# Optimization experiments

Measured on AMD Instinct MI355X. Metric: run time of the kernel, lower is better.

## Reference

```python
import jax, jax.numpy as jnp
import numpy as np

B, N, D = 128, 512, 256
NUM_TYPES, NUM_STATS = 6, 8
W_TYPE, W_STATS, W_CORR = 1.0, 1.0, 0.5
LN_EPS = 1e-5


def _mlp_head(x, W1, b1, g, be, W2, b2):
    # Linear -> GELU(exact) -> LayerNorm -> Linear (dropout is identity in eval)
    h = x @ W1 + b1
    h = jax.nn.gelu(h, approximate=False)
    mu = jnp.mean(h, axis=-1, keepdims=True)
    var = jnp.var(h, axis=-1, keepdims=True)
    h = (h - mu) / jnp.sqrt(var + LN_EPS) * g + be
    return h @ W2 + b2


def _masked_mean(x, m):
    m = m.astype(x.dtype)
    return jnp.sum(x * m) / jnp.maximum(jnp.sum(m), 1.0)


def setup_inputs() -> dict:
    key = jax.random.key(0)
    ks = jax.random.split(key, 16)
    s = 1.0 / np.sqrt(D)
    return {
        'column_embeddings': jax.random.normal(ks[0], (B, N, D), jnp.float32),
        'masked_columns': jax.random.uniform(ks[1], (B, N)) < 0.15,
        'type_targets': jax.random.randint(ks[2], (B, N), 0, NUM_TYPES),
        'column_statistics': jax.random.normal(ks[3], (B, N, NUM_STATS), jnp.float32),
        'column_correlations': jax.random.normal(ks[4], (B, N, N), jnp.float32),
        # type head params
        'Wt1': jax.random.normal(ks[5], (D, D), jnp.float32) * s,
        'bt1': jnp.zeros((D,), jnp.float32),
        'gt': jnp.ones((D,), jnp.float32),
        'blt': jnp.zeros((D,), jnp.float32),
        'Wt2': jax.random.normal(ks[6], (D, NUM_TYPES), jnp.float32) * s,
        'bt2': jnp.zeros((NUM_TYPES,), jnp.float32),
        # stats head params
        'Ws1': jax.random.normal(ks[7], (D, D), jnp.float32) * s,
        'bs1': jnp.zeros((D,), jnp.float32),
        'gs': jnp.ones((D,), jnp.float32),
        'bls': jnp.zeros((D,), jnp.float32),
        'Ws2': jax.random.normal(ks[8], (D, NUM_STATS), jnp.float32) * s,
        'bs2': jnp.zeros((NUM_STATS,), jnp.float32),
        # bilinear correlation head (nn.Bilinear(d,d,1) weight [1,d,d] -> [d,d])
        'Wc': jax.random.normal(ks[9], (D, D), jnp.float32) * s,
        'bc': jnp.zeros((), jnp.float32),
    }


def reference(column_embeddings, masked_columns, type_targets, column_statistics,
              column_correlations, Wt1, bt1, gt, blt, Wt2, bt2,
              Ws1, bs1, gs, bls, Ws2, bs2, Wc, bc):
    x = column_embeddings
    m = masked_columns

    type_logits = _mlp_head(x, Wt1, bt1, gt, blt, Wt2, bt2)   # [B,N,6]
    stats_preds = _mlp_head(x, Ws1, bs1, gs, bls, Ws2, bs2)   # [B,N,8]

    # fused bilinear correlation: replaces the O(N^2) python loop
    scores = jnp.einsum('bid,de,bje->bij', x, Wc, x) + bc     # [B,N,N]
    corr = jnp.tanh(scores)
    eye = jnp.eye(N, dtype=bool)
    corr = jnp.where(eye, jnp.ones((), corr.dtype), corr)

    # type loss: masked-mean cross-entropy
    logp = jax.nn.log_softmax(type_logits, axis=-1)
    nll = -jnp.take_along_axis(logp, type_targets[..., None], axis=-1)[..., 0]
    type_loss = _masked_mean(nll, m)

    # stats loss: masked-mean MSE over all stat elements of masked columns
    se = (stats_preds - column_statistics) ** 2
    stats_loss = _masked_mean(se, jnp.broadcast_to(m[:, :, None], se.shape))

    # correlation loss: mask is union over row/col masked columns
    m2 = m[:, :, None] | m[:, None, :]
    corr_loss = _masked_mean((corr - column_correlations) ** 2, m2)

    total = W_TYPE * type_loss + W_STATS * stats_loss + W_CORR * corr_loss
    return total
```

## Files before the change

kernel.cpp:

```cpp
#include <hip/hip_runtime.h>
#include <hip/hip_bf16.h>

#define BB 128
#define NN 512
#define DD 256

typedef __attribute__((ext_vector_type(4))) float f32x4;
typedef __attribute__((ext_vector_type(8))) short s16x8;
typedef __attribute__((ext_vector_type(8))) __bf16 bf16x8;

static __device__ __forceinline__ bf16x8 as_bf(s16x8 v) {
  return __builtin_bit_cast(bf16x8, v);
}

static __device__ __forceinline__ unsigned short f2bf(float f) {
  unsigned u = __builtin_bit_cast(unsigned, f);
  u += 0x7FFFu + ((u >> 16) & 1u);
  return (unsigned short)(u >> 16);
}

static __device__ __forceinline__ float gelu_fast(float h) {
  float z = 1.5957691216057308f * h * (1.0f + 0.044715f * h * h);
  float e = __expf(z);
  float r = __builtin_amdgcn_rcpf(e + 1.0f);
  return h - h * r;
}

__device__ __forceinline__ float wave_sum(float v) {
#pragma unroll
  for (int o = 32; o > 0; o >>= 1) v += __shfl_xor(v, o);
  return v;
}

__global__ void k_init(int* wsi) {
  if (threadIdx.x < 8) wsi[threadIdx.x] = 0;
}

__global__ void k_counts(const int* __restrict__ msk, int* __restrict__ wsi) {
  const int b = blockIdx.x;
  int cnt = 0;
  for (int i = threadIdx.x; i < NN; i += blockDim.x) cnt += (msk[b * NN + i] != 0) ? 1 : 0;
  float s = wave_sum((float)cnt);
  __shared__ float red[4];
  const int lane = threadIdx.x & 63, wv = threadIdx.x >> 6;
  if (lane == 0) red[wv] = s;
  __syncthreads();
  if (threadIdx.x == 0) {
    int k = (int)(red[0] + red[1] + red[2] + red[3] + 0.5f);
    atomicAdd(&wsi[4], k);
    atomicAdd(&wsi[5], NN * NN - (NN - k) * (NN - k));
  }
}

__global__ void k_prep(const float* __restrict__ Wc, const float* __restrict__ Wt1,
                       const float* __restrict__ Ws1, const float* __restrict__ Wt2,
                       const float* __restrict__ Ws2,
                       unsigned short* __restrict__ WcT, unsigned short* __restrict__ Wt1T,
                       unsigned short* __restrict__ Ws1T, unsigned short* __restrict__ Wt2T,
                       unsigned short* __restrict__ Ws2T) {
  int t = blockIdx.x * 256 + threadIdx.x;
  int c = t >> 8, d = t & 255;
  WcT [c * 256 + d] = f2bf(Wc [d * 256 + c]);
  Wt1T[c * 256 + d] = f2bf(Wt1[d * 256 + c]);
  Ws1T[c * 256 + d] = f2bf(Ws1[d * 256 + c]);
  if (c < 16) {
    Wt2T[c * 256 + d] = (c < 6) ? f2bf(Wt2[d * 6 + c]) : (unsigned short)0;
    Ws2T[c * 256 + d] = (c < 8) ? f2bf(Ws2[d * 8 + c]) : (unsigned short)0;
  }
}

__global__ __launch_bounds__(512) void k_heads(
    const float* __restrict__ x, unsigned short* __restrict__ xbf,
    const int* __restrict__ msk,
    const int* __restrict__ tgt, const float* __restrict__ stats,
    const unsigned short* __restrict__ Wt1T, const unsigned short* __restrict__ Ws1T,
    const unsigned short* __restrict__ Wt2T, const unsigned short* __restrict__ Ws2T,
    const float* __restrict__ bt1, const float* __restrict__ bs1,
    const float* __restrict__ gt, const float* __restrict__ gs,
    const float* __restrict__ blt, const float* __restrict__ bls,
    const float* __restrict__ bt2, const float* __restrict__ bs2,
    float* __restrict__ fs)
{
  const int tid = threadIdx.x;
  const int lane = tid & 63, w = tid >> 6;
  const int wm = w & 1, wn = w >> 1;
  const int fr = lane & 15, fg = lane >> 4;
  const int row0 = blockIdx.x * 128;

  __shared__ __align__(16) unsigned short lds_x[128 * 264];
  __shared__ __align__(16) unsigned short pool2[4224];
  __shared__ float lg[128 * 8];
  unsigned short* lds_h  = lds_x;
  unsigned short* lds_w2 = pool2;
  float* red = (float*)pool2;

#pragma unroll
  for (int p = 0; p < 8; ++p) {
    int c = tid + p * 512;
    int r = c >> 5, ch = c & 31;
    const float4* s = (const float4*)&x[(size_t)(row0 + r) * DD + ch * 8];
    float4 v0 = s[0], v1 = s[1];
    uint4 pk;
    pk.x = (unsigned)f2bf(v0.x) | ((unsigned)f2bf(v0.y) << 16);
    pk.y = (unsigned)f2bf(v0.z) | ((unsigned)f2bf(v0.w) << 16);
    pk.z = (unsigned)f2bf(v1.x) | ((unsigned)f2bf(v1.y) << 16);
    pk.w = (unsigned)f2bf(v1.z) | ((unsigned)f2bf(v1.w) << 16);
    *(uint4*)&lds_x[r * 264 + ch * 8] = pk;
    *(uint4*)&xbf[(size_t)(row0 + r) * DD + ch * 8] = pk;
  }
  __syncthreads();

  f32x4 at[4][4], asx[4][4];
#pragma unroll
  for (int i = 0; i < 4; ++i)
#pragma unroll
    for (int j = 0; j < 4; ++j) {
      at[i][j]  = f32x4{0.f, 0.f, 0.f, 0.f};
      asx[i][j] = f32x4{0.f, 0.f, 0.f, 0.f};
    }

#pragma unroll
  for (int ks = 0; ks < 8; ++ks) {
    const int ko = ks * 32 + fg * 8;
    s16x8 af[4], bt_[4], bs_[4];
#pragma unroll
    for (int i = 0; i < 4; ++i)
      af[i] = *(const s16x8*)&lds_x[(wm * 64 + i * 16 + fr) * 264 + ko];
#pragma unroll
    for (int j = 0; j < 4; ++j) {
      bt_[j] = *(const s16x8*)&Wt1T[(size_t)(wn * 64 + j * 16 + fr) * DD + ko];
      bs_[j] = *(const s16x8*)&Ws1T[(size_t)(wn * 64 + j * 16 + fr) * DD + ko];
    }
#pragma unroll
    for (int i = 0; i < 4; ++i)
#pragma unroll
      for (int j = 0; j < 4; ++j) {
        at[i][j]  = __builtin_amdgcn_mfma_f32_16x16x32_bf16(as_bf(af[i]), as_bf(bt_[j]), at[i][j], 0, 0, 0);
        asx[i][j] = __builtin_amdgcn_mfma_f32_16x16x32_bf16(as_bf(af[i]), as_bf(bs_[j]), asx[i][j], 0, 0, 0);
      }
  }

  {
    float sA[16], qA[16];
#pragma unroll
    for (int k = 0; k < 16; ++k) { sA[k] = 0.f; qA[k] = 0.f; }
#pragma unroll
    for (int i = 0; i < 4; ++i)
#pragma unroll
      for (int j = 0; j < 4; ++j) {
        int col = wn * 64 + j * 16 + fr;
        float bb = bt1[col];
#pragma unroll
        for (int r = 0; r < 4; ++r) {
          float h = gelu_fast(at[i][j][r] + bb);
          at[i][j][r] = h;
          sA[i * 4 + r] += h;
          qA[i * 4 + r] += h * h;
        }
      }
#pragma unroll
    for (int o = 1; o < 16; o <<= 1) {
#pragma unroll
      for (int k = 0; k < 16; ++k) {
        sA[k] += __shfl_xor(sA[k], o);
        qA[k] += __shfl_xor(qA[k], o);
      }
    }
    if (fr == 0) {
#pragma unroll
      for (int i = 0; i < 4; ++i)
#pragma unroll
        for (int r = 0; r < 4; ++r) {
          int row = wm * 64 + i * 16 + fg * 4 + r;
          red[row * 8 + wn]     = sA[i * 4 + r];
          red[row * 8 + 4 + wn] = qA[i * 4 + r];
        }
    }
    __syncthreads();
#pragma unroll
    for (int i = 0; i < 4; ++i)
#pragma unroll
      for (int r = 0; r < 4; ++r) {
        int row = wm * 64 + i * 16 + fg * 4 + r;
        float s = red[row * 8 + 0] + red[row * 8 + 1] + red[row * 8 + 2] + red[row * 8 + 3];
        float q = red[row * 8 + 4] + red[row * 8 + 5] + red[row * 8 + 6] + red[row * 8 + 7];
        float mu = s * (1.0f / DD);
        float var = q * (1.0f / DD) - mu * mu;
        float rstd = rsqrtf(var + 1e-5f);
#pragma unroll
        for (int j = 0; j < 4; ++j) {
          int col = wn * 64 + j * 16 + fr;
          float hn = (at[i][j][r] - mu) * rstd * gt[col] + blt[col];
          lds_h[row * 264 + col] = f2bf(hn);
        }
      }
    __syncthreads();
    {
      int r = tid >> 5, ch = tid & 31;
      *(uint4*)&lds_w2[r * 264 + ch * 8] = *(const uint4*)&Wt2T[r * 256 + ch * 8];
    }
    __syncthreads();
    {
      f32x4 a1 = f32x4{0.f, 0.f, 0.f, 0.f};
#pragma unroll
      for (int ks = 0; ks < 8; ++ks) {
        s16x8 av = *(const s16x8*)&lds_h[(w * 16 + fr) * 264 + ks * 32 + fg * 8];
        s16x8 bv = *(const s16x8*)&lds_w2[fr * 264 + ks * 32 + fg * 8];
        a1 = __builtin_amdgcn_mfma_f32_16x16x32_bf16(as_bf(av), as_bf(bv), a1, 0, 0, 0);
      }
      if (fr < 8) {
#pragma unroll
        for (int r = 0; r < 4; ++r) lg[(w * 16 + fg * 4 + r) * 8 + fr] = a1[r];
      }
    }
    __syncthreads();
    if (tid < 128) {
      int grow = row0 + tid;
      int mbit = msk[grow];
      float l[6], mx = -1e30f;
#pragma unroll
      for (int c = 0; c < 6; ++c) { l[c] = lg[tid * 8 + c] + bt2[c]; mx = fmaxf(mx, l[c]); }
      float se = 0.0f;
#pragma unroll
      for (int c = 0; c < 6; ++c) se += expf(l[c] - mx);
      float lse = mx + logf(se);
      int t = tgt[grow];
      float lt = 0.0f;
#pragma unroll
      for (int c = 0; c < 6; ++c) lt = (c == t) ? l[c] : lt;
      float contrib = mbit ? (lse - lt) : 0.0f;
      float s = wave_sum(contrib);
      if ((tid & 63) == 0) atomicAdd(&fs[0], s);
    }
    __syncthreads();
  }

  {
    float sA[16], qA[16];
#pragma unroll
    for (int k = 0; k < 16; ++k) { sA[k] = 0.f; qA[k] = 0.f; }
#pragma unroll
    for (int i = 0; i < 4; ++i)
#pragma unroll
      for (int j = 0; j < 4; ++j) {
        int col = wn * 64 + j * 16 + fr;
        float bb = bs1[col];
#pragma unroll
        for (int r = 0; r < 4; ++r) {
          float h = gelu_fast(asx[i][j][r] + bb);
          asx[i][j][r] = h;
          sA[i * 4 + r] += h;
          qA[i * 4 + r] += h * h;
        }
      }
#pragma unroll
    for (int o = 1; o < 16; o <<= 1) {
#pragma unroll
      for (int k = 0; k < 16; ++k) {
        sA[k] += __shfl_xor(sA[k], o);
        qA[k] += __shfl_xor(qA[k], o);
      }
    }
    if (fr == 0) {
#pragma unroll
      for (int i = 0; i < 4; ++i)
#pragma unroll
        for (int r = 0; r < 4; ++r) {
          int row = wm * 64 + i * 16 + fg * 4 + r;
          red[row * 8 + wn]     = sA[i * 4 + r];
          red[row * 8 + 4 + wn] = qA[i * 4 + r];
        }
    }
    __syncthreads();
#pragma unroll
    for (int i = 0; i < 4; ++i)
#pragma unroll
      for (int r = 0; r < 4; ++r) {
        int row = wm * 64 + i * 16 + fg * 4 + r;
        float s = red[row * 8 + 0] + red[row * 8 + 1] + red[row * 8 + 2] + red[row * 8 + 3];
        float q = red[row * 8 + 4] + red[row * 8 + 5] + red[row * 8 + 6] + red[row * 8 + 7];
        float mu = s * (1.0f / DD);
        float var = q * (1.0f / DD) - mu * mu;
        float rstd = rsqrtf(var + 1e-5f);
#pragma unroll
        for (int j = 0; j < 4; ++j) {
          int col = wn * 64 + j * 16 + fr;
          float hn = (asx[i][j][r] - mu) * rstd * gs[col] + bls[col];
          lds_h[row * 264 + col] = f2bf(hn);
        }
      }
    __syncthreads();
    {
      int r = tid >> 5, ch = tid & 31;
      *(uint4*)&lds_w2[r * 264 + ch * 8] = *(const uint4*)&Ws2T[r * 256 + ch * 8];
    }
    __syncthreads();
    {
      f32x4 a1 = f32x4{0.f, 0.f, 0.f, 0.f};
#pragma unroll
      for (int ks = 0; ks < 8; ++ks) {
        s16x8 av = *(const s16x8*)&lds_h[(w * 16 + fr) * 264 + ks * 32 + fg * 8];
        s16x8 bv = *(const s16x8*)&lds_w2[fr * 264 + ks * 32 + fg * 8];
        a1 = __builtin_amdgcn_mfma_f32_16x16x32_bf16(as_bf(av), as_bf(bv), a1, 0, 0, 0);
      }
      if (fr < 8) {
#pragma unroll
        for (int r = 0; r < 4; ++r) lg[(w * 16 + fg * 4 + r) * 8 + fr] = a1[r];
      }
    }
    __syncthreads();
    if (tid < 128) {
      int grow = row0 + tid;
      int mbit = msk[grow];
      const float* st = stats + (size_t)grow * 8;
      float sse = 0.0f;
#pragma unroll
      for (int c = 0; c < 8; ++c) {
        float d = (lg[tid * 8 + c] + bs2[c]) - st[c];
        sse += d * d;
      }
      float contrib = mbit ? sse : 0.0f;
      float s = wave_sum(contrib);
      if ((tid & 63) == 0) atomicAdd(&fs[1], s);
    }
  }
}

__global__ __launch_bounds__(512) void k_corr(
    const unsigned short* __restrict__ xbf, const int* __restrict__ msk,
    const float* __restrict__ corr, const unsigned short* __restrict__ WcT,
    const float* __restrict__ bcp, float* __restrict__ fs)
{
  const int tid = threadIdx.x;
  const int b  = blockIdx.x >> 3;
  const int it = blockIdx.x & 7;
  const int i0 = it * 64;
  const int lane = tid & 63, w = tid >> 6;
  const int wn = w;
  const int fr = lane & 15, fg = lane >> 4;

  __shared__ __align__(16) unsigned short lds_y[64 * 264];
  __shared__ __align__(16) unsigned short lds_a[64 * 72];
  __shared__ __align__(16) unsigned short lds_b[256 * 72];
  __shared__ int ms_i[64];
  __shared__ int ms_j[256];
  __shared__ float red8[8];

  const unsigned short* xb = xbf + (size_t)b * NN * DD;

  f32x4 acc[4][2];
#pragma unroll
  for (int i = 0; i < 4; ++i)
#pragma unroll
    for (int j = 0; j < 2; ++j) acc[i][j] = f32x4{0.f, 0.f, 0.f, 0.f};

  for (int kt = 0; kt < 4; ++kt) {
    __syncthreads();
    {
      int r = tid >> 3, ch = tid & 7;
      *(uint4*)&lds_a[r * 72 + ch * 8] = *(const uint4*)&xb[(size_t)(i0 + r) * DD + kt * 64 + ch * 8];
    }
#pragma unroll
    for (int p = 0; p < 4; ++p) {
      int idx = tid + p * 512;
      int r = idx >> 3, ch = idx & 7;
      *(uint4*)&lds_b[r * 72 + ch * 8] = *(const uint4*)&WcT[r * 256 + kt * 64 + ch * 8];
    }
    __syncthreads();
#pragma unroll
    for (int ks = 0; ks < 2; ++ks) {
      s16x8 af[4], bfv[2];
#pragma unroll
      for (int i = 0; i < 4; ++i)
        af[i] = *(const s16x8*)&lds_a[(i * 16 + fr) * 72 + ks * 32 + fg * 8];
#pragma unroll
      for (int j = 0; j < 2; ++j)
        bfv[j] = *(const s16x8*)&lds_b[(wn * 32 + j * 16 + fr) * 72 + ks * 32 + fg * 8];
#pragma unroll
      for (int i = 0; i < 4; ++i)
#pragma unroll
        for (int j = 0; j < 2; ++j)
          acc[i][j] = __builtin_amdgcn_mfma_f32_16x16x32_bf16(as_bf(af[i]), as_bf(bfv[j]), acc[i][j], 0, 0, 0);
    }
  }
#pragma unroll
  for (int i = 0; i < 4; ++i)
#pragma unroll
    for (int j = 0; j < 2; ++j)
#pragma unroll
      for (int r = 0; r < 4; ++r) {
        int row = i * 16 + fg * 4 + r;
        int col = wn * 32 + j * 16 + fr;
        lds_y[row * 264 + col] = f2bf(acc[i][j][r]);
      }
  if (tid < 64) ms_i[tid] = msk[b * NN + i0 + tid];

  const float bc = bcp[0];
  const float* tb = corr + (size_t)b * NN * NN;
  float sse = 0.0f;

  for (int jc = 0; jc < 2; ++jc) {
    const int j0 = jc * 256;
#pragma unroll
    for (int i = 0; i < 4; ++i)
#pragma unroll
      for (int j = 0; j < 2; ++j) acc[i][j] = f32x4{0.f, 0.f, 0.f, 0.f};

    for (int kt = 0; kt < 4; ++kt) {
      __syncthreads();
#pragma unroll
      for (int p = 0; p < 4; ++p) {
        int idx = tid + p * 512;
        int r = idx >> 3, ch = idx & 7;
        *(uint4*)&lds_b[r * 72 + ch * 8] = *(const uint4*)&xb[(size_t)(j0 + r) * DD + kt * 64 + ch * 8];
      }
      if (kt == 0 && tid < 256) ms_j[tid] = msk[b * NN + j0 + tid];
      __syncthreads();
#pragma unroll
      for (int ks = 0; ks < 2; ++ks) {
        s16x8 af[4], bfv[2];
#pragma unroll
        for (int i = 0; i < 4; ++i)
          af[i] = *(const s16x8*)&lds_y[(i * 16 + fr) * 264 + kt * 64 + ks * 32 + fg * 8];
#pragma unroll
        for (int j = 0; j < 2; ++j)
          bfv[j] = *(const s16x8*)&lds_b[(wn * 32 + j * 16 + fr) * 72 + ks * 32 + fg * 8];
#pragma unroll
        for (int i = 0; i < 4; ++i)
#pragma unroll
          for (int j = 0; j < 2; ++j)
            acc[i][j] = __builtin_amdgcn_mfma_f32_16x16x32_bf16(as_bf(af[i]), as_bf(bfv[j]), acc[i][j], 0, 0, 0);
      }
    }

    float tg[4][2][4];
#pragma unroll
    for (int i = 0; i < 4; ++i) {
      int rbase = i0 + i * 16 + fg * 4;
#pragma unroll
      for (int j = 0; j < 2; ++j) {
        int gj = j0 + wn * 32 + j * 16 + fr;
#pragma unroll
        for (int r = 0; r < 4; ++r)
          tg[i][j][r] = tb[(size_t)(rbase + r) * NN + gj];
      }
    }

#pragma unroll
    for (int i = 0; i < 4; ++i) {
      int rbase = i * 16 + fg * 4;
#pragma unroll
      for (int j = 0; j < 2; ++j) {
        int colc = wn * 32 + j * 16 + fr;
        int gj = j0 + colc;
        int mj = ms_j[colc];
#pragma unroll
        for (int r = 0; r < 4; ++r) {
          int gi = i0 + rbase + r;
          float s = acc[i][j][r] + bc;
          float e = __expf(2.0f * s);
          float cv = 1.0f - 2.0f * __builtin_amdgcn_rcpf(e + 1.0f);
          if (gi == gj) cv = 1.0f;
          float d = cv - tg[i][j][r];
          int mb = ms_i[rbase + r] | mj;
          sse += mb ? d * d : 0.0f;
        }
      }
    }
  }

  float s = wave_sum(sse);
  if (lane == 0) red8[w] = s;
  __syncthreads();
  if (tid == 0) {
    float t = 0.f;
#pragma unroll
    for (int i = 0; i < 8; ++i) t += red8[i];
    atomicAdd(&fs[2], t);
  }
}

__global__ void k_final(const float* __restrict__ fs, const int* __restrict__ wsi,
                        float* __restrict__ out) {
  if (threadIdx.x == 0 && blockIdx.x == 0) {
    float cm = (float)wsi[4];
    float c2 = (float)wsi[5];
    out[0] = fs[0] / fmaxf(cm, 1.0f) + fs[1] / fmaxf(8.0f * cm, 1.0f) +
             0.5f * fs[2] / fmaxf(c2, 1.0f);
  }
}

extern "C" void kernel_launch(void* const* d_in, const int* in_sizes, int n_in,
                              void* d_out, int out_size, void* d_ws, size_t ws_size,
                              hipStream_t stream) {
  const float* x     = (const float*)d_in[0];
  const int*   msk   = (const int*)d_in[1];
  const int*   tgt   = (const int*)d_in[2];
  const float* stats = (const float*)d_in[3];
  const float* corr  = (const float*)d_in[4];
  const float* Wt1   = (const float*)d_in[5];
  const float* bt1   = (const float*)d_in[6];
  const float* gt    = (const float*)d_in[7];
  const float* blt   = (const float*)d_in[8];
  const float* Wt2   = (const float*)d_in[9];
  const float* bt2   = (const float*)d_in[10];
  const float* Ws1   = (const float*)d_in[11];
  const float* bs1   = (const float*)d_in[12];
  const float* gs    = (const float*)d_in[13];
  const float* bls   = (const float*)d_in[14];
  const float* Ws2   = (const float*)d_in[15];
  const float* bs2   = (const float*)d_in[16];
  const float* Wc    = (const float*)d_in[17];
  const float* bc    = (const float*)d_in[18];

  float* fs = (float*)d_ws;
  int* wsi  = (int*)d_ws;
  unsigned short* WcT  = (unsigned short*)((char*)d_ws + 256);
  unsigned short* Wt1T = WcT + 65536;
  unsigned short* Ws1T = Wt1T + 65536;
  unsigned short* Wt2T = Ws1T + 65536;
  unsigned short* Ws2T = Wt2T + 4096;
  unsigned short* xbf  = Ws2T + 4096;

  hipLaunchKernelGGL(k_init, dim3(1), dim3(64), 0, stream, wsi);
  hipLaunchKernelGGL(k_counts, dim3(BB), dim3(256), 0, stream, msk, wsi);
  hipLaunchKernelGGL(k_prep, dim3(256), dim3(256), 0, stream,
                     Wc, Wt1, Ws1, Wt2, Ws2, WcT, Wt1T, Ws1T, Wt2T, Ws2T);
  hipLaunchKernelGGL(k_heads, dim3((BB * NN) / 128), dim3(512), 0, stream,
                     x, xbf, msk, tgt, stats, Wt1T, Ws1T, Wt2T, Ws2T,
                     bt1, bs1, gt, gs, blt, bls, bt2, bs2, fs);
  hipLaunchKernelGGL(k_corr, dim3(BB * (NN / 64)), dim3(512), 0, stream,
                     xbf, msk, corr, WcT, bc, fs);
  hipLaunchKernelGGL(k_final, dim3(1), dim3(64), 0, stream, fs, wsi, (float*)d_out);
}
```

Baseline: 172.9 us.

## Merge MLP heads and bilinear correlation into one kernel, drop bf16 x buffer

Fuses the two MLP heads and the correlation kernel into a single kernel, one block per 64 rows of a batch. The x@Wc projection is computed alongside the head GEMMs from the same LDS tile, and the intermediate bf16 copy of x is no longer written to global memory. The j-side operand is now loaded as fp32 from x and converted in-kernel, which doubles its read bytes and repeats the conversion per block. It saves one launch and the xbf round trip, but raises LDS and register use, which may lower occupancy.

```diff
diff --git a/kernel.cpp b/kernel.cpp
--- a/kernel.cpp
+++ b/kernel.cpp
@@ -69,33 +69,42 @@
   }
 }
 
-__global__ __launch_bounds__(512) void k_heads(
-    const float* __restrict__ x, unsigned short* __restrict__ xbf,
-    const int* __restrict__ msk,
+__global__ __launch_bounds__(512) void k_merged(
+    const float* __restrict__ x, const int* __restrict__ msk,
     const int* __restrict__ tgt, const float* __restrict__ stats,
+    const float* __restrict__ corr,
+    const unsigned short* __restrict__ WcT,
     const unsigned short* __restrict__ Wt1T, const unsigned short* __restrict__ Ws1T,
     const unsigned short* __restrict__ Wt2T, const unsigned short* __restrict__ Ws2T,
     const float* __restrict__ bt1, const float* __restrict__ bs1,
     const float* __restrict__ gt, const float* __restrict__ gs,
     const float* __restrict__ blt, const float* __restrict__ bls,
     const float* __restrict__ bt2, const float* __restrict__ bs2,
-    float* __restrict__ fs)
+    const float* __restrict__ bcp, float* __restrict__ fs)
 {
   const int tid = threadIdx.x;
+  const int b  = blockIdx.x >> 3;
+  const int it = blockIdx.x & 7;
+  const int i0 = it * 64;
   const int lane = tid & 63, w = tid >> 6;
-  const int wm = w & 1, wn = w >> 1;
+  const int wm = w & 1, wn4 = w >> 1;
+  const int wn8 = w;
   const int fr = lane & 15, fg = lane >> 4;
-  const int row0 = blockIdx.x * 128;
-
-  __shared__ __align__(16) unsigned short lds_x[128 * 264];
+  const int row0 = b * NN + i0;
+
+  __shared__ __align__(16) unsigned short lds_xy[64 * 264];
+  __shared__ __align__(16) unsigned short lds_jb[256 * 72];
   __shared__ __align__(16) unsigned short pool2[4224];
-  __shared__ float lg[128 * 8];
-  unsigned short* lds_h  = lds_x;
+  __shared__ float lg[64 * 8];
+  __shared__ int ms_i[64];
+  __shared__ int ms_j[256];
+  __shared__ float red8[8];
+  unsigned short* lds_h  = lds_jb;
   unsigned short* lds_w2 = pool2;
   float* red = (float*)pool2;
 
 #pragma unroll
-  for (int p = 0; p < 8; ++p) {
+  for (int p = 0; p < 4; ++p) {
     int c = tid + p * 512;
     int r = c >> 5, ch = c & 31;
     const float4* s = (const float4*)&x[(size_t)(row0 + r) * DD + ch * 8];
@@ -105,50 +114,65 @@
     pk.y = (unsigned)f2bf(v0.z) | ((unsigned)f2bf(v0.w) << 16);
     pk.z = (unsigned)f2bf(v1.x) | ((unsigned)f2bf(v1.y) << 16);
     pk.w = (unsigned)f2bf(v1.z) | ((unsigned)f2bf(v1.w) << 16);
-    *(uint4*)&lds_x[r * 264 + ch * 8] = pk;
-    *(uint4*)&xbf[(size_t)(row0 + r) * DD + ch * 8] = pk;
+    *(uint4*)&lds_xy[r * 264 + ch * 8] = pk;
   }
   __syncthreads();
 
-  f32x4 at[4][4], asx[4][4];
-#pragma unroll
-  for (int i = 0; i < 4; ++i)
+  f32x4 at[2][4], asx[2][4], ay[2][4];
+#pragma unroll
+  for (int i = 0; i < 2; ++i)
 #pragma unroll
     for (int j = 0; j < 4; ++j) {
       at[i][j]  = f32x4{0.f, 0.f, 0.f, 0.f};
       asx[i][j] = f32x4{0.f, 0.f, 0.f, 0.f};
+      ay[i][j]  = f32x4{0.f, 0.f, 0.f, 0.f};
     }
 
 #pragma unroll
   for (int ks = 0; ks < 8; ++ks) {
     const int ko = ks * 32 + fg * 8;
-    s16x8 af[4], bt_[4], bs_[4];
-#pragma unroll
-    for (int i = 0; i < 4; ++i)
-      af[i] = *(const s16x8*)&lds_x[(wm * 64 + i * 16 + fr) * 264 + ko];
+    s16x8 af[2], bt_[4], bs_[4], bc_[4];
+#pragma unroll
+    for (int i = 0; i < 2; ++i)
+      af[i] = *(const s16x8*)&lds_xy[(wm * 32 + i * 16 + fr) * 264 + ko];
 #pragma unroll
     for (int j = 0; j < 4; ++j) {
-      bt_[j] = *(const s16x8*)&Wt1T[(size_t)(wn * 64 + j * 16 + fr) * DD + ko];
-      bs_[j] = *(const s16x8*)&Ws1T[(size_t)(wn * 64 + j * 16 + fr) * DD + ko];
-    }
-#pragma unroll
-    for (int i = 0; i < 4; ++i)
+      bt_[j] = *(const s16x8*)&Wt1T[(size_t)(wn4 * 64 + j * 16 + fr) * DD + ko];
+      bs_[j] = *(const s16x8*)&Ws1T[(size_t)(wn4 * 64 + j * 16 + fr) * DD + ko];
+      bc_[j] = *(const s16x8*)&WcT [(size_t)(wn4 * 64 + j * 16 + fr) * DD + ko];
+    }
+#pragma unroll
+    for (int i = 0; i < 2; ++i)
 #pragma unroll
       for (int j = 0; j < 4; ++j) {
         at[i][j]  = __builtin_amdgcn_mfma_f32_16x16x32_bf16(as_bf(af[i]), as_bf(bt_[j]), at[i][j], 0, 0, 0);
         asx[i][j] = __builtin_amdgcn_mfma_f32_16x16x32_bf16(as_bf(af[i]), as_bf(bs_[j]), asx[i][j], 0, 0, 0);
-      }
-  }
+        ay[i][j]  = __builtin_amdgcn_mfma_f32_16x16x32_bf16(as_bf(af[i]), as_bf(bc_[j]), ay[i][j], 0, 0, 0);
+      }
+  }
+  __syncthreads();
+
+#pragma unroll
+  for (int i = 0; i < 2; ++i)
+#pragma unroll
+    for (int j = 0; j < 4; ++j)
+#pragma unroll
+      for (int r = 0; r < 4; ++r) {
+        int row = wm * 32 + i * 16 + fg * 4 + r;
+        int col = wn4 * 64 + j * 16 + fr;
+        lds_xy[row * 264 + col] = f2bf(ay[i][j][r]);
+      }
+  if (tid < 64) ms_i[tid] = msk[row0 + tid];
 
   {
-    float sA[16], qA[16];
-#pragma unroll
-    for (int k = 0; k < 16; ++k) { sA[k] = 0.f; qA[k] = 0.f; }
-#pragma unroll
-    for (int i = 0; i < 4; ++i)
+    float sA[8], qA[8];
+#pragma unroll
+    for (int k = 0; k < 8; ++k) { sA[k] = 0.f; qA[k] = 0.f; }
+#pragma unroll
+    for (int i = 0; i < 2; ++i)
 #pragma unroll
       for (int j = 0; j < 4; ++j) {
-        int col = wn * 64 + j * 16 + fr;
+        int col = wn4 * 64 + j * 16 + fr;
         float bb = bt1[col];
 #pragma unroll
         for (int r = 0; r < 4; ++r) {
@@ -161,27 +185,27 @@
 #pragma unroll
     for (int o = 1; o < 16; o <<= 1) {
 #pragma unroll
-      for (int k = 0; k < 16; ++k) {
+      for (int k = 0; k < 8; ++k) {
         sA[k] += __shfl_xor(sA[k], o);
         qA[k] += __shfl_xor(qA[k], o);
       }
     }
     if (fr == 0) {
 #pragma unroll
-      for (int i = 0; i < 4; ++i)
+      for (int i = 0; i < 2; ++i)
 #pragma unroll
         for (int r = 0; r < 4; ++r) {
-          int row = wm * 64 + i * 16 + fg * 4 + r;
-          red[row * 8 + wn]     = sA[i * 4 + r];
-          red[row * 8 + 4 + wn] = qA[i * 4 + r];
-        }
-    }
-    __syncthreads();
-#pragma unroll
-    for (int i = 0; i < 4; ++i)
+          int row = wm * 32 + i * 16 + fg * 4 + r;
+          red[row * 8 + wn4]     = sA[i * 4 + r];
+          red[row * 8 + 4 + wn4] = qA[i * 4 + r];
+        }
+    }
+    __syncthreads();
+#pragma unroll
+    for (int i = 0; i < 2; ++i)
 #pragma unroll
       for (int r = 0; r < 4; ++r) {
-        int row = wm * 64 + i * 16 + fg * 4 + r;
+        int row = wm * 32 + i * 16 + fg * 4 + r;
         float s = red[row * 8 + 0] + red[row * 8 + 1] + red[row * 8 + 2] + red[row * 8 + 3];
         float q = red[row * 8 + 4] + red[row * 8 + 5] + red[row * 8 + 6] + red[row * 8 + 7];
         float mu = s * (1.0f / DD);
@@ -189,7 +213,7 @@
         float rstd = rsqrtf(var + 1e-5f);
 #pragma unroll
         for (int j = 0; j < 4; ++j) {
-          int col = wn * 64 + j * 16 + fr;
+          int col = wn4 * 64 + j * 16 + fr;
           float hn = (at[i][j][r] - mu) * rstd * gt[col] + blt[col];
           lds_h[row * 264 + col] = f2bf(hn);
         }
@@ -200,7 +224,7 @@
       *(uint4*)&lds_w2[r * 264 + ch * 8] = *(const uint4*)&Wt2T[r * 256 + ch * 8];
     }
     __syncthreads();
-    {
+    if (w < 4) {
       f32x4 a1 = f32x4{0.f, 0.f, 0.f, 0.f};
 #pragma unroll
       for (int ks = 0; ks < 8; ++ks) {
@@ -214,7 +238,7 @@
       }
     }
     __syncthreads();
-    if (tid < 128) {
+    if (tid < 64) {
       int grow = row0 + tid;
       int mbit = msk[grow];
       float l[6], mx = -1e30f;
@@ -230,20 +254,20 @@
       for (int c = 0; c < 6; ++c) lt = (c == t) ? l[c] : lt;
       float contrib = mbit ? (lse - lt) : 0.0f;
       float s = wave_sum(contrib);
-      if ((tid & 63) == 0) atomicAdd(&fs[0], s);
+      if (tid == 0) atomicAdd(&fs[0], s);
     }
     __syncthreads();
   }
 
   {
-    float sA[16], qA[16];
-#pragma unroll
-    for (int k = 0; k < 16; ++k) { sA[k] = 0.f; qA[k] = 0.f; }
-#pragma unroll
-    for (int i = 0; i < 4; ++i)
+    float sA[8], qA[8];
+#pragma unroll
+    for (int k = 0; k < 8; ++k) { sA[k] = 0.f; qA[k] = 0.f; }
+#pragma unroll
+    for (int i = 0; i < 2; ++i)
 #pragma unroll
       for (int j = 0; j < 4; ++j) {
-        int col = wn * 64 + j * 16 + fr;
+        int col = wn4 * 64 + j * 16 + fr;
         float bb = bs1[col];
 #pragma unroll
         for (int r = 0; r < 4; ++r) {
@@ -256,27 +280,27 @@
 #pragma unroll
     for (int o = 1; o < 16; o <<= 1) {
 #pragma unroll
-      for (int k = 0; k < 16; ++k) {
+      for (int k = 0; k < 8; ++k) {
         sA[k] += __shfl_xor(sA[k], o);
         qA[k] += __shfl_xor(qA[k], o);
       }
     }
     if (fr == 0) {
 #pragma unroll
-      for (int i = 0; i < 4; ++i)
+      for (int i = 0; i < 2; ++i)
 #pragma unroll
         for (int r = 0; r < 4; ++r) {
-          int row = wm * 64 + i * 16 + fg * 4 + r;
-          red[row * 8 + wn]     = sA[i * 4 + r];
-          red[row * 8 + 4 + wn] = qA[i * 4 + r];
-        }
-    }
-    __syncthreads();
-#pragma unroll
-    for (int i = 0; i < 4; ++i)
+          int row = wm * 32 + i * 16 + fg * 4 + r;
+          red[row * 8 + wn4]     = sA[i * 4 + r];
+          red[row * 8 + 4 + wn4] = qA[i * 4 + r];
+        }
+    }
+    __syncthreads();
+#pragma unroll
+    for (int i = 0; i < 2; ++i)
 #pragma unroll
       for (int r = 0; r < 4; ++r) {
-        int row = wm * 64 + i * 16 + fg * 4 + r;
+        int row = wm * 32 + i * 16 + fg * 4 + r;
         float s = red[row * 8 + 0] + red[row * 8 + 1] + red[row * 8 + 2] + red[row * 8 + 3];
         float q = red[row * 8 + 4] + red[row * 8 + 5] + red[row * 8 + 6] + red[row * 8 + 7];
         float mu = s * (1.0f / DD);
@@ -284,7 +308,7 @@
         float rstd = rsqrtf(var + 1e-5f);
 #pragma unroll
         for (int j = 0; j < 4; ++j) {
-          int col = wn * 64 + j * 16 + fr;
+          int col = wn4 * 64 + j * 16 + fr;
           float hn = (asx[i][j][r] - mu) * rstd * gs[col] + bls[col];
           lds_h[row * 264 + col] = f2bf(hn);
         }
@@ -295,7 +319,7 @@
       *(uint4*)&lds_w2[r * 264 + ch * 8] = *(const uint4*)&Ws2T[r * 256 + ch * 8];
     }
     __syncthreads();
-    {
+    if (w < 4) {
       f32x4 a1 = f32x4{0.f, 0.f, 0.f, 0.f};
 #pragma unroll
       for (int ks = 0; ks < 8; ++ks) {
@@ -309,7 +333,7 @@
       }
     }
     __syncthreads();
-    if (tid < 128) {
+    if (tid < 64) {
       int grow = row0 + tid;
       int mbit = msk[grow];
       const float* st = stats + (size_t)grow * 8;
@@ -321,83 +345,16 @@
       }
       float contrib = mbit ? sse : 0.0f;
       float s = wave_sum(contrib);
-      if ((tid & 63) == 0) atomicAdd(&fs[1], s);
-    }
-  }
-}
-
-__global__ __launch_bounds__(512) void k_corr(
-    const unsigned short* __restrict__ xbf, const int* __restrict__ msk,
-    const float* __restrict__ corr, const unsigned short* __restrict__ WcT,
-    const float* __restrict__ bcp, float* __restrict__ fs)
-{
-  const int tid = threadIdx.x;
-  const int b  = blockIdx.x >> 3;
-  const int it = blockIdx.x & 7;
-  const int i0 = it * 64;
-  const int lane = tid & 63, w = tid >> 6;
-  const int wn = w;
-  const int fr = lane & 15, fg = lane >> 4;
-
-  __shared__ __align__(16) unsigned short lds_y[64 * 264];
-  __shared__ __align__(16) unsigned short lds_a[64 * 72];
-  __shared__ __align__(16) unsigned short lds_b[256 * 72];
-  __shared__ int ms_i[64];
-  __shared__ int ms_j[256];
-  __shared__ float red8[8];
-
-  const unsigned short* xb = xbf + (size_t)b * NN * DD;
-
-  f32x4 acc[4][2];
-#pragma unroll
-  for (int i = 0; i < 4; ++i)
-#pragma unroll
-    for (int j = 0; j < 2; ++j) acc[i][j] = f32x4{0.f, 0.f, 0.f, 0.f};
-
-  for (int kt = 0; kt < 4; ++kt) {
-    __syncthreads();
-    {
-      int r = tid >> 3, ch = tid & 7;
-      *(uint4*)&lds_a[r * 72 + ch * 8] = *(const uint4*)&xb[(size_t)(i0 + r) * DD + kt * 64 + ch * 8];
-    }
-#pragma unroll
-    for (int p = 0; p < 4; ++p) {
-      int idx = tid + p * 512;
-      int r = idx >> 3, ch = idx & 7;
-      *(uint4*)&lds_b[r * 72 + ch * 8] = *(const uint4*)&WcT[r * 256 + kt * 64 + ch * 8];
-    }
-    __syncthreads();
-#pragma unroll
-    for (int ks = 0; ks < 2; ++ks) {
-      s16x8 af[4], bfv[2];
-#pragma unroll
-      for (int i = 0; i < 4; ++i)
-        af[i] = *(const s16x8*)&lds_a[(i * 16 + fr) * 72 + ks * 32 + fg * 8];
-#pragma unroll
-      for (int j = 0; j < 2; ++j)
-        bfv[j] = *(const s16x8*)&lds_b[(wn * 32 + j * 16 + fr) * 72 + ks * 32 + fg * 8];
-#pragma unroll
-      for (int i = 0; i < 4; ++i)
-#pragma unroll
-        for (int j = 0; j < 2; ++j)
-          acc[i][j] = __builtin_amdgcn_mfma_f32_16x16x32_bf16(as_bf(af[i]), as_bf(bfv[j]), acc[i][j], 0, 0, 0);
-    }
-  }
-#pragma unroll
-  for (int i = 0; i < 4; ++i)
-#pragma unroll
-    for (int j = 0; j < 2; ++j)
-#pragma unroll
-      for (int r = 0; r < 4; ++r) {
-        int row = i * 16 + fg * 4 + r;
-        int col = wn * 32 + j * 16 + fr;
-        lds_y[row * 264 + col] = f2bf(acc[i][j][r]);
-      }
-  if (tid < 64) ms_i[tid] = msk[b * NN + i0 + tid];
+      if (tid == 0) atomicAdd(&fs[1], s);
+    }
+    __syncthreads();
+  }
 
   const float bc = bcp[0];
   const float* tb = corr + (size_t)b * NN * NN;
+  const float* xb32 = x + (size_t)b * NN * DD;
   float sse = 0.0f;
+  f32x4 acc[4][2];
 
   for (int jc = 0; jc < 2; ++jc) {
     const int j0 = jc * 256;
@@ -412,7 +369,14 @@
       for (int p = 0; p < 4; ++p) {
         int idx = tid + p * 512;
         int r = idx >> 3, ch = idx & 7;
-        *(uint4*)&lds_b[r * 72 + ch * 8] = *(const uint4*)&xb[(size_t)(j0 + r) * DD + kt * 64 + ch * 8];
+        const float4* s = (const float4*)&xb32[(size_t)(j0 + r) * DD + kt * 64 + ch * 8];
+        float4 v0 = s[0], v1 = s[1];
+        uint4 pk;
+        pk.x = (unsigned)f2bf(v0.x) | ((unsigned)f2bf(v0.y) << 16);
+        pk.y = (unsigned)f2bf(v0.z) | ((unsigned)f2bf(v0.w) << 16);
+        pk.z = (unsigned)f2bf(v1.x) | ((unsigned)f2bf(v1.y) << 16);
+        pk.w = (unsigned)f2bf(v1.z) | ((unsigned)f2bf(v1.w) << 16);
+        *(uint4*)&lds_jb[r * 72 + ch * 8] = pk;
       }
       if (kt == 0 && tid < 256) ms_j[tid] = msk[b * NN + j0 + tid];
       __syncthreads();
@@ -421,10 +385,10 @@
         s16x8 af[4], bfv[2];
 #pragma unroll
         for (int i = 0; i < 4; ++i)
-          af[i] = *(const s16x8*)&lds_y[(i * 16 + fr) * 264 + kt * 64 + ks * 32 + fg * 8];
+          af[i] = *(const s16x8*)&lds_xy[(i * 16 + fr) * 264 + kt * 64 + ks * 32 + fg * 8];
 #pragma unroll
         for (int j = 0; j < 2; ++j)
-          bfv[j] = *(const s16x8*)&lds_b[(wn * 32 + j * 16 + fr) * 72 + ks * 32 + fg * 8];
+          bfv[j] = *(const s16x8*)&lds_jb[(wn8 * 32 + j * 16 + fr) * 72 + ks * 32 + fg * 8];
 #pragma unroll
         for (int i = 0; i < 4; ++i)
 #pragma unroll
@@ -439,7 +403,7 @@
       int rbase = i0 + i * 16 + fg * 4;
 #pragma unroll
       for (int j = 0; j < 2; ++j) {
-        int gj = j0 + wn * 32 + j * 16 + fr;
+        int gj = j0 + wn8 * 32 + j * 16 + fr;
 #pragma unroll
         for (int r = 0; r < 4; ++r)
           tg[i][j][r] = tb[(size_t)(rbase + r) * NN + gj];
@@ -451,7 +415,7 @@
       int rbase = i * 16 + fg * 4;
 #pragma unroll
       for (int j = 0; j < 2; ++j) {
-        int colc = wn * 32 + j * 16 + fr;
+        int colc = wn8 * 32 + j * 16 + fr;
         int gj = j0 + colc;
         int mj = ms_j[colc];
 #pragma unroll
@@ -520,16 +484,13 @@
   unsigned short* Ws1T = Wt1T + 65536;
   unsigned short* Wt2T = Ws1T + 65536;
   unsigned short* Ws2T = Wt2T + 4096;
-  unsigned short* xbf  = Ws2T + 4096;
 
   hipLaunchKernelGGL(k_init, dim3(1), dim3(64), 0, stream, wsi);
   hipLaunchKernelGGL(k_counts, dim3(BB), dim3(256), 0, stream, msk, wsi);
   hipLaunchKernelGGL(k_prep, dim3(256), dim3(256), 0, stream,
                      Wc, Wt1, Ws1, Wt2, Ws2, WcT, Wt1T, Ws1T, Wt2T, Ws2T);
-  hipLaunchKernelGGL(k_heads, dim3((BB * NN) / 128), dim3(512), 0, stream,
-                     x, xbf, msk, tgt, stats, Wt1T, Ws1T, Wt2T, Ws2T,
-                     bt1, bs1, gt, gs, blt, bls, bt2, bs2, fs);
-  hipLaunchKernelGGL(k_corr, dim3(BB * (NN / 64)), dim3(512), 0, stream,
-                     xbf, msk, corr, WcT, bc, fs);
+  hipLaunchKernelGGL(k_merged, dim3(BB * (NN / 64)), dim3(512), 0, stream,
+                     x, msk, tgt, stats, corr, WcT, Wt1T, Ws1T, Wt2T, Ws2T,
+                     bt1, bs1, gt, gs, blt, bls, bt2, bs2, bc, fs);
   hipLaunchKernelGGL(k_final, dim3(1), dim3(64), 0, stream, fs, wsi, (float*)d_out);
 }
```

New measurement: 245.1 us. +41.7%, slower.
